# Performance work log

Hardware: AMD Instinct MI355X
Metric: run time of the kernel (lower is better)

Reference implementation:

```python
import jax, jax.numpy as jnp
import numpy as np

N_DIMS = 64
N_HALF = N_DIMS // 2
HIDDEN = 512
N_LAYERS = 8
BATCH = 16384

IDX_EVEN = np.arange(0, N_DIMS, 2)  # mask != 0 for even layers
IDX_ODD = np.arange(1, N_DIMS, 2)


def _init_mlp_params(key, n_in, n_hidden, n_out, n_layers):
    ks = jax.random.split(key, 3)
    def lin(k, fi, fo):
        return jax.random.normal(k, (n_layers, fi, fo), dtype=jnp.float32) / np.sqrt(fi)
    W1 = lin(ks[0], n_in, n_hidden)
    W2 = lin(ks[1], n_hidden, n_hidden)
    W3 = lin(ks[2], n_hidden, n_out)
    b1 = jnp.zeros((n_layers, n_hidden), jnp.float32)
    b2 = jnp.zeros((n_layers, n_hidden), jnp.float32)
    b3 = jnp.zeros((n_layers, n_out), jnp.float32)
    return W1, b1, W2, b2, W3, b3


def setup_inputs() -> dict:
    key = jax.random.key(0)
    ky, kt, ks = jax.random.split(key, 3)
    y = jax.random.normal(ky, (BATCH, N_DIMS), dtype=jnp.float32)
    tW1, tb1, tW2, tb2, tW3, tb3 = _init_mlp_params(kt, N_HALF, HIDDEN, N_HALF, N_LAYERS)
    sW1, sb1, sW2, sb2, sW3, sb3 = _init_mlp_params(ks, N_HALF, HIDDEN, N_HALF, N_LAYERS)
    s_scale = jnp.ones((N_LAYERS, N_HALF), jnp.float32)
    s_shift = jnp.zeros((N_LAYERS, N_HALF), jnp.float32)
    return {
        "y": y,
        "tW1": tW1, "tb1": tb1, "tW2": tW2, "tb2": tb2, "tW3": tW3, "tb3": tb3,
        "sW1": sW1, "sb1": sb1, "sW2": sW2, "sb2": sb2, "sW3": sW3, "sb3": sb3,
        "s_scale": s_scale, "s_shift": s_shift,
    }


def _mlp(x, W1, b1, W2, b2, W3, b3):
    h = jax.nn.relu(x @ W1 + b1)
    h = jax.nn.relu(h @ W2 + b2)
    return h @ W3 + b3


def reference(y, tW1, tb1, tW2, tb2, tW3, tb3,
              sW1, sb1, sW2, sb2, sW3, sb3, s_scale, s_shift):
    z = y
    log_det = jnp.zeros_like(y)
    for i in range(N_LAYERS):
        i0 = IDX_EVEN if i % 2 == 0 else IDX_ODD  # transformed half
        i1 = IDX_ODD if i % 2 == 0 else IDX_EVEN  # conditioning half
        z0 = z[:, i0]  # [B, 32]
        z1 = z[:, i1]  # [B, 32]
        t = _mlp(z1, tW1[i], tb1[i], tW2[i], tb2[i], tW3[i], tb3[i])
        s = jnp.tanh(_mlp(z1, sW1[i], sb1[i], sW2[i], sb2[i], sW3[i], sb3[i])) * s_scale[i] + s_shift[i]
        z0 = z0 * jnp.exp(s) + t
        z = z.at[:, i0].set(z0)
        log_det = log_det.at[:, i0].add(s)
    return z, log_det
```

## Files before the change

kernel.cpp:

```cpp
#include <hip/hip_runtime.h>

typedef unsigned short u16;
typedef unsigned int   u32;
typedef _Float16 f16;
typedef __attribute__((ext_vector_type(8))) _Float16 half8;
typedef __attribute__((ext_vector_type(4))) float f32x4;

#define NBATCH 16384

__device__ __forceinline__ u16 f2h(float x) {
  union { f16 h; u16 u; } v; v.h = (f16)x; return v.u;
}

__global__ __launch_bounds__(256) void cvt_all(
    const float* __restrict__ tW1, const float* __restrict__ sW1,
    const float* __restrict__ tW2, const float* __restrict__ sW2,
    const float* __restrict__ tW3, const float* __restrict__ sW3,
    u16* __restrict__ dW1, u16* __restrict__ dW2, u16* __restrict__ dW3)
{
  __shared__ float tile[32][33];
  const int z = blockIdx.z, bx = blockIdx.x;
  const float *tsrc, *ssrc; u16* dst; int M, N, nt, mt;
  if (bx < 16)       { tsrc = tW1; ssrc = sW1; dst = dW1; M = 32;  N = 512; nt = bx;           mt = 0; }
  else if (bx < 272) { tsrc = tW2; ssrc = sW2; dst = dW2; M = 512; N = 512; nt = (bx - 16) & 15; mt = (bx - 16) >> 4; }
  else               { tsrc = tW3; ssrc = sW3; dst = dW3; M = 512; N = 32;  nt = 0;            mt = bx - 272; }
  const float* src = ((z & 1) ? ssrc : tsrc) + (size_t)(z >> 1) * M * N;
  u16* d = dst + (size_t)z * M * N;
  const int n0 = nt * 32, m0 = mt * 32;
  for (int r = 0; r < 4; r++) {
    int m = m0 + threadIdx.y + r * 8, n = n0 + threadIdx.x;
    tile[threadIdx.y + r * 8][threadIdx.x] = src[(size_t)m * N + n];
  }
  __syncthreads();
  for (int r = 0; r < 4; r++) {
    int n = n0 + threadIdx.y + r * 8, m = m0 + threadIdx.x;
    d[(size_t)n * M + m] = f2h(tile[threadIdx.x][threadIdx.y + r * 8]);
  }
}

__global__ __launch_bounds__(512, 2) void meganvp(
    const float* __restrict__ y,
    const u16* __restrict__ W1T, const u16* __restrict__ W2T, const u16* __restrict__ W3T,
    const float* __restrict__ tb1, const float* __restrict__ sb1,
    const float* __restrict__ tb2, const float* __restrict__ sb2,
    const float* __restrict__ tb3, const float* __restrict__ sb3,
    const float* __restrict__ s_scale, const float* __restrict__ s_shift,
    float* __restrict__ out)
{
  __shared__ u16 bufA[64 * 512];
  __shared__ u16 bufB[64 * 512];
  __shared__ u16 X[64 * 40];
  __shared__ float TS[64 * 68];

  const int t = threadIdx.x;
  const int m0 = blockIdx.x * 64;
  const int lane = t & 63, w = t >> 6, lm = lane & 15, quad = lane >> 4;
  const int cw = w * 64;
  const int phase = blockIdx.x & 15;
  const int zr = t >> 3, zq = t & 7, c0 = zq * 8;

  float z[8], ld[8];
  {
    const float* yb = y + (size_t)(m0 + zr) * 64 + c0;
    f32x4 v0 = *(const f32x4*)&yb[0];
    f32x4 v1 = *(const f32x4*)&yb[4];
#pragma unroll
    for (int k = 0; k < 4; k++) { z[k] = v0[k]; z[4 + k] = v1[k]; }
#pragma unroll
    for (int e = 0; e < 8; e++) ld[e] = 0.f;
  }

  for (int layer = 0; layer < 8; layer++) {
    const int par = layer & 1;
    {
      union { u16 a[4]; uint2 v; } xv;
#pragma unroll
      for (int e = 0; e < 4; e++) xv.a[e] = f2h(z[2 * e + 1 - par]);
      *(uint2*)&X[zr * 40 + zq * 4] = xv.v;
    }
    __syncthreads();

    for (int net = 0; net < 2; net++) {
      const int idx = layer * 2 + net;

      {
        const float* b1p = (net ? sb1 : tb1) + layer * 512 + cw + quad * 4;
        f32x4 bias1[4];
#pragma unroll
        for (int ct = 0; ct < 4; ct++) bias1[ct] = *(const f32x4*)&b1p[ct * 16];
        const u16* W1p = W1T + ((size_t)idx * 512 + cw + lm) * 32 + quad * 8;
        half8 bv[4];
#pragma unroll
        for (int ct = 0; ct < 4; ct++) bv[ct] = *(const half8*)&W1p[ct * 512];
        half8 av[4];
#pragma unroll
        for (int rt = 0; rt < 4; rt++)
          av[rt] = *(const half8*)&X[(rt * 16 + lm) * 40 + quad * 8];
        f32x4 zz = {0.f, 0.f, 0.f, 0.f};
        f32x4 acc[4][4];
#pragma unroll
        for (int rt = 0; rt < 4; rt++)
#pragma unroll
          for (int ct = 0; ct < 4; ct++)
            acc[rt][ct] = __builtin_amdgcn_mfma_f32_16x16x32_f16(bv[ct], av[rt], zz, 0, 0, 0);
#pragma unroll
        for (int rt = 0; rt < 4; rt++) {
          const int m = rt * 16 + lm;
#pragma unroll
          for (int ct = 0; ct < 4; ct++) {
            const int n0 = cw + ct * 16 + quad * 4;
            union { u16 a[4]; uint2 v; } pk;
#pragma unroll
            for (int g = 0; g < 4; g++) {
              float v = acc[rt][ct][g] + bias1[ct][g];
              pk.a[g] = f2h(v > 0.f ? v : 0.f);
            }
            *(uint2*)&bufA[m * 512 + ((((n0 >> 3) ^ (m & 7)) << 3) | (n0 & 7))] = pk.v;
          }
        }
      }
      __syncthreads();

      {
        const float* b2p = (net ? sb2 : tb2) + layer * 512 + cw + quad * 4;
        f32x4 bias2[4];
#pragma unroll
        for (int ct = 0; ct < 4; ct++) bias2[ct] = *(const f32x4*)&b2p[ct * 16];
        const u16* W2p = W2T + ((size_t)idx * 512 + cw + lm) * 512 + quad * 8;
        f32x4 zz = {0.f, 0.f, 0.f, 0.f};
        f32x4 acc[4][4];
#pragma unroll
        for (int rt = 0; rt < 4; rt++)
#pragma unroll
          for (int ct = 0; ct < 4; ct++) acc[rt][ct] = zz;
        half8 bb[3][4];
#pragma unroll
        for (int p = 0; p < 3; p++) {
          const int kp = ((p + phase) & 15) * 32;
#pragma unroll
          for (int ct = 0; ct < 4; ct++)
            bb[p][ct] = *(const half8*)&W2p[ct * 8192 + kp];
        }
#pragma unroll
        for (int ci = 0; ci < 16; ci++) {
          const int kk = ((ci + phase) & 15) * 32;
          half8 av[4];
#pragma unroll
          for (int rt = 0; rt < 4; rt++) {
            const int m = rt * 16 + lm;
            av[rt] = *(const half8*)&bufA[m * 512 + ((((kk >> 3) + quad) ^ (m & 7)) << 3)];
          }
#pragma unroll
          for (int rt = 0; rt < 4; rt++)
#pragma unroll
            for (int ct = 0; ct < 4; ct++)
              acc[rt][ct] = __builtin_amdgcn_mfma_f32_16x16x32_f16(bb[ci % 3][ct], av[rt], acc[rt][ct], 0, 0, 0);
          if (ci < 13) {
            const int kn = ((ci + 3 + phase) & 15) * 32;
#pragma unroll
            for (int ct = 0; ct < 4; ct++)
              bb[ci % 3][ct] = *(const half8*)&W2p[ct * 8192 + kn];
          }
        }
#pragma unroll
        for (int rt = 0; rt < 4; rt++) {
          const int m = rt * 16 + lm;
#pragma unroll
          for (int ct = 0; ct < 4; ct++) {
            const int n0 = cw + ct * 16 + quad * 4;
            union { u16 a[4]; uint2 v; } pk;
#pragma unroll
            for (int g = 0; g < 4; g++) {
              float v = acc[rt][ct][g] + bias2[ct][g];
              pk.a[g] = f2h(v > 0.f ? v : 0.f);
            }
            *(uint2*)&bufB[m * 512 + ((((n0 >> 3) ^ (m & 7)) << 3) | (n0 & 7))] = pk.v;
          }
        }
      }
      __syncthreads();

      {
        const int hr = (w & 3) * 16, hc = (w >> 2) * 16;
        const u16* W3p = W3T + ((size_t)idx * 32 + hc + lm) * 512 + quad * 8;
        f32x4 ha[2];
        ha[0] = (f32x4){0.f, 0.f, 0.f, 0.f}; ha[1] = ha[0];
        const int m = hr + lm;
        half8 pv[4];
#pragma unroll
        for (int p = 0; p < 4; p++)
          pv[p] = *(const half8*)&W3p[((p + phase) & 15) * 32];
#pragma unroll
        for (int ci = 0; ci < 16; ci++) {
          const int kk = ((ci + phase) & 15) * 32;
          half8 av = *(const half8*)&bufB[m * 512 + ((((kk >> 3) + quad) ^ (m & 7)) << 3)];
          ha[ci & 1] = __builtin_amdgcn_mfma_f32_16x16x32_f16(pv[ci & 3], av, ha[ci & 1], 0, 0, 0);
          if (ci < 12)
            pv[ci & 3] = *(const half8*)&W3p[((ci + 4 + phase) & 15) * 32];
        }
        const int j0 = hc + quad * 4;
        if (net == 0) {
          const f32x4 b3 = *(const f32x4*)&tb3[layer * 32 + j0];
#pragma unroll
          for (int g = 0; g < 4; g++)
            TS[m * 68 + 2 * (j0 + g)] = ha[0][g] + ha[1][g] + b3[g];
        } else {
          const f32x4 b3 = *(const f32x4*)&sb3[layer * 32 + j0];
          const f32x4 sc = *(const f32x4*)&s_scale[layer * 32 + j0];
          const f32x4 sh = *(const f32x4*)&s_shift[layer * 32 + j0];
#pragma unroll
          for (int g = 0; g < 4; g++)
            TS[m * 68 + 2 * (j0 + g) + 1] = tanhf(ha[0][g] + ha[1][g] + b3[g]) * sc[g] + sh[g];
        }
      }
      __syncthreads();
    }

    {
      const float* base = &TS[zr * 68 + zq * 8];
      f32x4 q0 = *(const f32x4*)&base[0];
      f32x4 q1 = *(const f32x4*)&base[4];
      float q[8];
#pragma unroll
      for (int k = 0; k < 4; k++) { q[k] = q0[k]; q[4 + k] = q1[k]; }
#pragma unroll
      for (int e = 0; e < 4; e++) {
        const float tv = q[2 * e], sv = q[2 * e + 1];
        const int zi = 2 * e + par;
        z[zi] = z[zi] * expf(sv) + tv;
        ld[zi] += sv;
      }
    }
  }

  {
    float* zb = out + (size_t)(m0 + zr) * 64 + c0;
    float* lb = out + (size_t)NBATCH * 64 + (size_t)(m0 + zr) * 64 + c0;
    f32x4 v0, v1, l0, l1;
#pragma unroll
    for (int k = 0; k < 4; k++) {
      v0[k] = z[k]; v1[k] = z[4 + k];
      l0[k] = ld[k]; l1[k] = ld[4 + k];
    }
    *(f32x4*)&zb[0] = v0; *(f32x4*)&zb[4] = v1;
    *(f32x4*)&lb[0] = l0; *(f32x4*)&lb[4] = l1;
  }
}

extern "C" void kernel_launch(void* const* d_in, const int* in_sizes, int n_in,
                              void* d_out, int out_size, void* d_ws, size_t ws_size,
                              hipStream_t stream) {
  (void)in_sizes; (void)n_in; (void)out_size; (void)ws_size;
  const float* y   = (const float*)d_in[0];
  const float* tW1 = (const float*)d_in[1];
  const float* tb1 = (const float*)d_in[2];
  const float* tW2 = (const float*)d_in[3];
  const float* tb2 = (const float*)d_in[4];
  const float* tW3 = (const float*)d_in[5];
  const float* tb3 = (const float*)d_in[6];
  const float* sW1 = (const float*)d_in[7];
  const float* sb1 = (const float*)d_in[8];
  const float* sW2 = (const float*)d_in[9];
  const float* sb2 = (const float*)d_in[10];
  const float* sW3 = (const float*)d_in[11];
  const float* sb3 = (const float*)d_in[12];
  const float* s_scale = (const float*)d_in[13];
  const float* s_shift = (const float*)d_in[14];
  float* out = (float*)d_out;

  char* ws = (char*)d_ws;
  const size_t W1SZ = (size_t)16 * 512 * 32 * 2;
  const size_t W2SZ = (size_t)16 * 512 * 512 * 2;
  u16* W1 = (u16*)(ws);
  u16* W2 = (u16*)(ws + W1SZ);
  u16* W3 = (u16*)(ws + W1SZ + W2SZ);

  cvt_all<<<dim3(288, 1, 16), dim3(32, 8), 0, stream>>>(tW1, sW1, tW2, sW2, tW3, sW3,
                                                        W1, W2, W3);

  meganvp<<<256, 512, 0, stream>>>(y, W1, W2, W3, tb1, sb1, tb2, sb2, tb3, sb3,
                                   s_scale, s_shift, out);
}
```

Baseline: 436.3 us.

## Switch hidden-layer GEMMs to 32x32x16 MFMA and double-buffer LDS operand loads

Replaces the 16x16x32 MFMA tiling in the first two MLP layers with 32x32x16 MFMA tiles, which changes the register fragment layout, the bias indexing and the swizzled LDS writeback. The larger tile is meant to reduce the number of LDS operand reads per FLOP. The LDS activation loads in the second and third GEMMs are now prefetched one k-step ahead into double buffers so they overlap with the MFMAs. The larger f32x16 accumulators and the extra buffers raise register pressure, which could cause spills or lower occupancy under launch_bounds(512,2).

```diff
diff --git a/kernel.cpp b/kernel.cpp
--- a/kernel.cpp
+++ b/kernel.cpp
@@ -5,6 +5,7 @@
 typedef _Float16 f16;
 typedef __attribute__((ext_vector_type(8))) _Float16 half8;
 typedef __attribute__((ext_vector_type(4))) float f32x4;
+typedef __attribute__((ext_vector_type(16))) float f32x16;
 
 #define NBATCH 16384
 
@@ -55,6 +56,7 @@
   const int t = threadIdx.x;
   const int m0 = blockIdx.x * 64;
   const int lane = t & 63, w = t >> 6, lm = lane & 15, quad = lane >> 4;
+  const int l31 = lane & 31, lh = lane >> 5;
   const int cw = w * 64;
   const int phase = blockIdx.x & 15;
   const int zr = t >> 3, zq = t & 7, c0 = zq * 8;
@@ -84,98 +86,129 @@
       const int idx = layer * 2 + net;
 
       {
-        const float* b1p = (net ? sb1 : tb1) + layer * 512 + cw + quad * 4;
-        f32x4 bias1[4];
-#pragma unroll
-        for (int ct = 0; ct < 4; ct++) bias1[ct] = *(const f32x4*)&b1p[ct * 16];
-        const u16* W1p = W1T + ((size_t)idx * 512 + cw + lm) * 32 + quad * 8;
-        half8 bv[4];
-#pragma unroll
-        for (int ct = 0; ct < 4; ct++) bv[ct] = *(const half8*)&W1p[ct * 512];
-        half8 av[4];
-#pragma unroll
-        for (int rt = 0; rt < 4; rt++)
-          av[rt] = *(const half8*)&X[(rt * 16 + lm) * 40 + quad * 8];
-        f32x4 zz = {0.f, 0.f, 0.f, 0.f};
-        f32x4 acc[4][4];
-#pragma unroll
-        for (int rt = 0; rt < 4; rt++)
-#pragma unroll
-          for (int ct = 0; ct < 4; ct++)
-            acc[rt][ct] = __builtin_amdgcn_mfma_f32_16x16x32_f16(bv[ct], av[rt], zz, 0, 0, 0);
-#pragma unroll
-        for (int rt = 0; rt < 4; rt++) {
-          const int m = rt * 16 + lm;
-#pragma unroll
-          for (int ct = 0; ct < 4; ct++) {
-            const int n0 = cw + ct * 16 + quad * 4;
-            union { u16 a[4]; uint2 v; } pk;
-#pragma unroll
-            for (int g = 0; g < 4; g++) {
-              float v = acc[rt][ct][g] + bias1[ct][g];
-              pk.a[g] = f2h(v > 0.f ? v : 0.f);
+        const u16* W1p = W1T + ((size_t)idx * 512 + cw + l31) * 32 + lh * 8;
+        half8 wv[2][2], xv[2][2];
+#pragma unroll
+        for (int ct = 0; ct < 2; ct++)
+#pragma unroll
+          for (int kh = 0; kh < 2; kh++)
+            wv[ct][kh] = *(const half8*)&W1p[ct * 1024 + kh * 16];
+#pragma unroll
+        for (int rt = 0; rt < 2; rt++)
+#pragma unroll
+          for (int kh = 0; kh < 2; kh++)
+            xv[rt][kh] = *(const half8*)&X[(rt * 32 + l31) * 40 + kh * 16 + lh * 8];
+        f32x16 zz;
+#pragma unroll
+        for (int i = 0; i < 16; i++) zz[i] = 0.f;
+        f32x16 acc1[2][2];
+#pragma unroll
+        for (int rt = 0; rt < 2; rt++)
+#pragma unroll
+          for (int ct = 0; ct < 2; ct++) {
+            acc1[rt][ct] = __builtin_amdgcn_mfma_f32_32x32x16_f16(wv[ct][0], xv[rt][0], zz, 0, 0, 0);
+            acc1[rt][ct] = __builtin_amdgcn_mfma_f32_32x32x16_f16(wv[ct][1], xv[rt][1], acc1[rt][ct], 0, 0, 0);
+          }
+        const float* b1g = (net ? sb1 : tb1) + layer * 512;
+#pragma unroll
+        for (int rt = 0; rt < 2; rt++) {
+          const int m = rt * 32 + l31;
+#pragma unroll
+          for (int ct = 0; ct < 2; ct++)
+#pragma unroll
+            for (int g8 = 0; g8 < 4; g8++) {
+              const int n0 = cw + ct * 32 + lh * 4 + g8 * 8;
+              const f32x4 bias = *(const f32x4*)&b1g[n0];
+              union { u16 a[4]; uint2 v; } pk;
+#pragma unroll
+              for (int g = 0; g < 4; g++) {
+                float v = acc1[rt][ct][g8 * 4 + g] + bias[g];
+                pk.a[g] = f2h(v > 0.f ? v : 0.f);
+              }
+              *(uint2*)&bufA[m * 512 + ((((n0 >> 3) ^ (m & 7)) << 3) | (n0 & 7))] = pk.v;
             }
-            *(uint2*)&bufA[m * 512 + ((((n0 >> 3) ^ (m & 7)) << 3) | (n0 & 7))] = pk.v;
-          }
         }
       }
       __syncthreads();
 
       {
-        const float* b2p = (net ? sb2 : tb2) + layer * 512 + cw + quad * 4;
-        f32x4 bias2[4];
-#pragma unroll
-        for (int ct = 0; ct < 4; ct++) bias2[ct] = *(const f32x4*)&b2p[ct * 16];
-        const u16* W2p = W2T + ((size_t)idx * 512 + cw + lm) * 512 + quad * 8;
-        f32x4 zz = {0.f, 0.f, 0.f, 0.f};
-        f32x4 acc[4][4];
-#pragma unroll
-        for (int rt = 0; rt < 4; rt++)
-#pragma unroll
-          for (int ct = 0; ct < 4; ct++) acc[rt][ct] = zz;
+        const u16* W2p = W2T + ((size_t)idx * 512 + cw + l31) * 512 + lh * 8;
+        f32x16 acc[2][2];
+#pragma unroll
+        for (int rt = 0; rt < 2; rt++)
+#pragma unroll
+          for (int ct = 0; ct < 2; ct++)
+#pragma unroll
+            for (int i = 0; i < 16; i++) acc[rt][ct][i] = 0.f;
         half8 bb[3][4];
 #pragma unroll
         for (int p = 0; p < 3; p++) {
           const int kp = ((p + phase) & 15) * 32;
 #pragma unroll
-          for (int ct = 0; ct < 4; ct++)
-            bb[p][ct] = *(const half8*)&W2p[ct * 8192 + kp];
+          for (int ct = 0; ct < 2; ct++)
+#pragma unroll
+            for (int kh = 0; kh < 2; kh++)
+              bb[p][ct * 2 + kh] = *(const half8*)&W2p[ct * 16384 + kp + kh * 16];
+        }
+        half8 av[2][4];
+        {
+          const int kk0 = (phase & 15) * 32;
+#pragma unroll
+          for (int rt = 0; rt < 2; rt++)
+#pragma unroll
+            for (int kh = 0; kh < 2; kh++) {
+              const int m = rt * 32 + l31;
+              const int c = (kk0 >> 3) + kh * 2 + lh;
+              av[0][rt * 2 + kh] = *(const half8*)&bufA[m * 512 + ((c ^ (m & 7)) << 3)];
+            }
         }
 #pragma unroll
         for (int ci = 0; ci < 16; ci++) {
-          const int kk = ((ci + phase) & 15) * 32;
-          half8 av[4];
-#pragma unroll
-          for (int rt = 0; rt < 4; rt++) {
-            const int m = rt * 16 + lm;
-            av[rt] = *(const half8*)&bufA[m * 512 + ((((kk >> 3) + quad) ^ (m & 7)) << 3)];
+          if (ci < 15) {
+            const int kk1 = ((ci + 1 + phase) & 15) * 32;
+#pragma unroll
+            for (int rt = 0; rt < 2; rt++)
+#pragma unroll
+              for (int kh = 0; kh < 2; kh++) {
+                const int m = rt * 32 + l31;
+                const int c = (kk1 >> 3) + kh * 2 + lh;
+                av[(ci + 1) & 1][rt * 2 + kh] = *(const half8*)&bufA[m * 512 + ((c ^ (m & 7)) << 3)];
+              }
           }
 #pragma unroll
-          for (int rt = 0; rt < 4; rt++)
-#pragma unroll
-            for (int ct = 0; ct < 4; ct++)
-              acc[rt][ct] = __builtin_amdgcn_mfma_f32_16x16x32_f16(bb[ci % 3][ct], av[rt], acc[rt][ct], 0, 0, 0);
+          for (int rt = 0; rt < 2; rt++)
+#pragma unroll
+            for (int ct = 0; ct < 2; ct++) {
+              acc[rt][ct] = __builtin_amdgcn_mfma_f32_32x32x16_f16(bb[ci % 3][ct * 2 + 0], av[ci & 1][rt * 2 + 0], acc[rt][ct], 0, 0, 0);
+              acc[rt][ct] = __builtin_amdgcn_mfma_f32_32x32x16_f16(bb[ci % 3][ct * 2 + 1], av[ci & 1][rt * 2 + 1], acc[rt][ct], 0, 0, 0);
+            }
           if (ci < 13) {
             const int kn = ((ci + 3 + phase) & 15) * 32;
 #pragma unroll
-            for (int ct = 0; ct < 4; ct++)
-              bb[ci % 3][ct] = *(const half8*)&W2p[ct * 8192 + kn];
+            for (int ct = 0; ct < 2; ct++)
+#pragma unroll
+              for (int kh = 0; kh < 2; kh++)
+                bb[ci % 3][ct * 2 + kh] = *(const half8*)&W2p[ct * 16384 + kn + kh * 16];
           }
         }
-#pragma unroll
-        for (int rt = 0; rt < 4; rt++) {
-          const int m = rt * 16 + lm;
-#pragma unroll
-          for (int ct = 0; ct < 4; ct++) {
-            const int n0 = cw + ct * 16 + quad * 4;
-            union { u16 a[4]; uint2 v; } pk;
-#pragma unroll
-            for (int g = 0; g < 4; g++) {
-              float v = acc[rt][ct][g] + bias2[ct][g];
-              pk.a[g] = f2h(v > 0.f ? v : 0.f);
+        const float* b2g = (net ? sb2 : tb2) + layer * 512;
+#pragma unroll
+        for (int rt = 0; rt < 2; rt++) {
+          const int m = rt * 32 + l31;
+#pragma unroll
+          for (int ct = 0; ct < 2; ct++)
+#pragma unroll
+            for (int g8 = 0; g8 < 4; g8++) {
+              const int n0 = cw + ct * 32 + lh * 4 + g8 * 8;
+              const f32x4 bias = *(const f32x4*)&b2g[n0];
+              union { u16 a[4]; uint2 v; } pk;
+#pragma unroll
+              for (int g = 0; g < 4; g++) {
+                float v = acc[rt][ct][g8 * 4 + g] + bias[g];
+                pk.a[g] = f2h(v > 0.f ? v : 0.f);
+              }
+              *(uint2*)&bufB[m * 512 + ((((n0 >> 3) ^ (m & 7)) << 3) | (n0 & 7))] = pk.v;
             }
-            *(uint2*)&bufB[m * 512 + ((((n0 >> 3) ^ (m & 7)) << 3) | (n0 & 7))] = pk.v;
-          }
         }
       }
       __syncthreads();
@@ -190,11 +223,18 @@
 #pragma unroll
         for (int p = 0; p < 4; p++)
           pv[p] = *(const half8*)&W3p[((p + phase) & 15) * 32];
+        half8 avh[2];
+        {
+          const int kk0 = (phase & 15) * 32;
+          avh[0] = *(const half8*)&bufB[m * 512 + ((((kk0 >> 3) + quad) ^ (m & 7)) << 3)];
+        }
 #pragma unroll
         for (int ci = 0; ci < 16; ci++) {
-          const int kk = ((ci + phase) & 15) * 32;
-          half8 av = *(const half8*)&bufB[m * 512 + ((((kk >> 3) + quad) ^ (m & 7)) << 3)];
-          ha[ci & 1] = __builtin_amdgcn_mfma_f32_16x16x32_f16(pv[ci & 3], av, ha[ci & 1], 0, 0, 0);
+          if (ci < 15) {
+            const int kk1 = ((ci + 1 + phase) & 15) * 32;
+            avh[(ci + 1) & 1] = *(const half8*)&bufB[m * 512 + ((((kk1 >> 3) + quad) ^ (m & 7)) << 3)];
+          }
+          ha[ci & 1] = __builtin_amdgcn_mfma_f32_16x16x32_f16(pv[ci & 3], avh[ci & 1], ha[ci & 1], 0, 0, 0);
           if (ci < 12)
             pv[ci & 3] = *(const half8*)&W3p[((ci + 4 + phase) & 15) * 32];
         }
```

Result: slower. 463.3 us (+6.2%).

## Prefetch next-stage weights before barriers and fuse head with next net's first layer

Applied to the files above, without the earlier changes.

Restructures the per-layer schedule so the W2 and W3 register prefetches are issued before each barrier, letting global loads overlap the sync wait. The t-net head is merged with the s-net first hidden layer in one barrier phase, removing one __syncthreads per layer. Biases are folded into the MFMA accumulator initialisation instead of being added afterwards. The cost is higher register pressure from the prefetch buffers staying live across phases, which could lower occupancy or cause spills.

```diff
diff --git a/kernel.cpp b/kernel.cpp
--- a/kernel.cpp
+++ b/kernel.cpp
@@ -58,6 +58,7 @@
   const int cw = w * 64;
   const int phase = blockIdx.x & 15;
   const int zr = t >> 3, zq = t & 7, c0 = zq * 8;
+  const int hr = (w & 3) * 16, hc = (w >> 2) * 16;
 
   float z[8], ld[8];
   {
@@ -70,6 +71,142 @@
     for (int e = 0; e < 8; e++) ld[e] = 0.f;
   }
 
+  half8 bb[3][4];
+  half8 pv[4];
+
+  auto BBPREF = [&](int idx) {
+    const u16* W2p = W2T + ((size_t)idx * 512 + cw + lm) * 512 + quad * 8;
+#pragma unroll
+    for (int p = 0; p < 3; p++) {
+      const int kp = ((p + phase) & 15) * 32;
+#pragma unroll
+      for (int ct = 0; ct < 4; ct++)
+        bb[p][ct] = *(const half8*)&W2p[ct * 8192 + kp];
+    }
+  };
+  auto PVPREF = [&](int idx) {
+    const u16* W3p = W3T + ((size_t)idx * 32 + hc + lm) * 512 + quad * 8;
+#pragma unroll
+    for (int p = 0; p < 4; p++)
+      pv[p] = *(const half8*)&W3p[((p + phase) & 15) * 32];
+  };
+
+  auto H1 = [&](int layer, int net) {
+    const int idx = layer * 2 + net;
+    const float* b1p = (net ? sb1 : tb1) + layer * 512 + cw + quad * 4;
+    f32x4 bias1[4];
+#pragma unroll
+    for (int ct = 0; ct < 4; ct++) bias1[ct] = *(const f32x4*)&b1p[ct * 16];
+    const u16* W1p = W1T + ((size_t)idx * 512 + cw + lm) * 32 + quad * 8;
+    half8 bv[4];
+#pragma unroll
+    for (int ct = 0; ct < 4; ct++) bv[ct] = *(const half8*)&W1p[ct * 512];
+    half8 av[4];
+#pragma unroll
+    for (int rt = 0; rt < 4; rt++)
+      av[rt] = *(const half8*)&X[(rt * 16 + lm) * 40 + quad * 8];
+    f32x4 acc[4][4];
+#pragma unroll
+    for (int rt = 0; rt < 4; rt++)
+#pragma unroll
+      for (int ct = 0; ct < 4; ct++)
+        acc[rt][ct] = __builtin_amdgcn_mfma_f32_16x16x32_f16(bv[ct], av[rt], bias1[ct], 0, 0, 0);
+#pragma unroll
+    for (int rt = 0; rt < 4; rt++) {
+      const int m = rt * 16 + lm;
+#pragma unroll
+      for (int ct = 0; ct < 4; ct++) {
+        const int n0 = cw + ct * 16 + quad * 4;
+        union { u16 a[4]; uint2 v; } pk;
+#pragma unroll
+        for (int g = 0; g < 4; g++) {
+          float v = acc[rt][ct][g];
+          pk.a[g] = f2h(v > 0.f ? v : 0.f);
+        }
+        *(uint2*)&bufA[m * 512 + ((((n0 >> 3) ^ (m & 7)) << 3) | (n0 & 7))] = pk.v;
+      }
+    }
+  };
+
+  auto H2 = [&](int layer, int net) {
+    const int idx = layer * 2 + net;
+    const float* b2p = (net ? sb2 : tb2) + layer * 512 + cw + quad * 4;
+    f32x4 acc[4][4];
+#pragma unroll
+    for (int ct = 0; ct < 4; ct++) {
+      const f32x4 b = *(const f32x4*)&b2p[ct * 16];
+#pragma unroll
+      for (int rt = 0; rt < 4; rt++) acc[rt][ct] = b;
+    }
+    const u16* W2p = W2T + ((size_t)idx * 512 + cw + lm) * 512 + quad * 8;
+#pragma unroll
+    for (int ci = 0; ci < 16; ci++) {
+      const int kk = ((ci + phase) & 15) * 32;
+      half8 av[4];
+#pragma unroll
+      for (int rt = 0; rt < 4; rt++) {
+        const int m = rt * 16 + lm;
+        av[rt] = *(const half8*)&bufA[m * 512 + ((((kk >> 3) + quad) ^ (m & 7)) << 3)];
+      }
+#pragma unroll
+      for (int rt = 0; rt < 4; rt++)
+#pragma unroll
+        for (int ct = 0; ct < 4; ct++)
+          acc[rt][ct] = __builtin_amdgcn_mfma_f32_16x16x32_f16(bb[ci % 3][ct], av[rt], acc[rt][ct], 0, 0, 0);
+      if (ci < 13) {
+        const int kn = ((ci + 3 + phase) & 15) * 32;
+#pragma unroll
+        for (int ct = 0; ct < 4; ct++)
+          bb[ci % 3][ct] = *(const half8*)&W2p[ct * 8192 + kn];
+      }
+    }
+#pragma unroll
+    for (int rt = 0; rt < 4; rt++) {
+      const int m = rt * 16 + lm;
+#pragma unroll
+      for (int ct = 0; ct < 4; ct++) {
+        const int n0 = cw + ct * 16 + quad * 4;
+        union { u16 a[4]; uint2 v; } pk;
+#pragma unroll
+        for (int g = 0; g < 4; g++) {
+          float v = acc[rt][ct][g];
+          pk.a[g] = f2h(v > 0.f ? v : 0.f);
+        }
+        *(uint2*)&bufB[m * 512 + ((((n0 >> 3) ^ (m & 7)) << 3) | (n0 & 7))] = pk.v;
+      }
+    }
+  };
+
+  auto HEAD = [&](int layer, int net) {
+    const int idx = layer * 2 + net;
+    const u16* W3p = W3T + ((size_t)idx * 32 + hc + lm) * 512 + quad * 8;
+    const int j0 = hc + quad * 4;
+    f32x4 ha[2];
+    ha[0] = net ? *(const f32x4*)&sb3[layer * 32 + j0]
+                : *(const f32x4*)&tb3[layer * 32 + j0];
+    ha[1] = (f32x4){0.f, 0.f, 0.f, 0.f};
+    const int m = hr + lm;
+#pragma unroll
+    for (int ci = 0; ci < 16; ci++) {
+      const int kk = ((ci + phase) & 15) * 32;
+      half8 av = *(const half8*)&bufB[m * 512 + ((((kk >> 3) + quad) ^ (m & 7)) << 3)];
+      ha[ci & 1] = __builtin_amdgcn_mfma_f32_16x16x32_f16(pv[ci & 3], av, ha[ci & 1], 0, 0, 0);
+      if (ci < 12)
+        pv[ci & 3] = *(const half8*)&W3p[((ci + 4 + phase) & 15) * 32];
+    }
+    if (net == 0) {
+#pragma unroll
+      for (int g = 0; g < 4; g++)
+        TS[m * 68 + 2 * (j0 + g)] = ha[0][g] + ha[1][g];
+    } else {
+      const f32x4 sc = *(const f32x4*)&s_scale[layer * 32 + j0];
+      const f32x4 sh = *(const f32x4*)&s_shift[layer * 32 + j0];
+#pragma unroll
+      for (int g = 0; g < 4; g++)
+        TS[m * 68 + 2 * (j0 + g) + 1] = tanhf(ha[0][g] + ha[1][g]) * sc[g] + sh[g];
+    }
+  };
+
   for (int layer = 0; layer < 8; layer++) {
     const int par = layer & 1;
     {
@@ -80,141 +217,25 @@
     }
     __syncthreads();
 
-    for (int net = 0; net < 2; net++) {
-      const int idx = layer * 2 + net;
-
-      {
-        const float* b1p = (net ? sb1 : tb1) + layer * 512 + cw + quad * 4;
-        f32x4 bias1[4];
-#pragma unroll
-        for (int ct = 0; ct < 4; ct++) bias1[ct] = *(const f32x4*)&b1p[ct * 16];
-        const u16* W1p = W1T + ((size_t)idx * 512 + cw + lm) * 32 + quad * 8;
-        half8 bv[4];
-#pragma unroll
-        for (int ct = 0; ct < 4; ct++) bv[ct] = *(const half8*)&W1p[ct * 512];
-        half8 av[4];
-#pragma unroll
-        for (int rt = 0; rt < 4; rt++)
-          av[rt] = *(const half8*)&X[(rt * 16 + lm) * 40 + quad * 8];
-        f32x4 zz = {0.f, 0.f, 0.f, 0.f};
-        f32x4 acc[4][4];
-#pragma unroll
-        for (int rt = 0; rt < 4; rt++)
-#pragma unroll
-          for (int ct = 0; ct < 4; ct++)
-            acc[rt][ct] = __builtin_amdgcn_mfma_f32_16x16x32_f16(bv[ct], av[rt], zz, 0, 0, 0);
-#pragma unroll
-        for (int rt = 0; rt < 4; rt++) {
-          const int m = rt * 16 + lm;
-#pragma unroll
-          for (int ct = 0; ct < 4; ct++) {
-            const int n0 = cw + ct * 16 + quad * 4;
-            union { u16 a[4]; uint2 v; } pk;
-#pragma unroll
-            for (int g = 0; g < 4; g++) {
-              float v = acc[rt][ct][g] + bias1[ct][g];
-              pk.a[g] = f2h(v > 0.f ? v : 0.f);
-            }
-            *(uint2*)&bufA[m * 512 + ((((n0 >> 3) ^ (m & 7)) << 3) | (n0 & 7))] = pk.v;
-          }
-        }
-      }
-      __syncthreads();
-
-      {
-        const float* b2p = (net ? sb2 : tb2) + layer * 512 + cw + quad * 4;
-        f32x4 bias2[4];
-#pragma unroll
-        for (int ct = 0; ct < 4; ct++) bias2[ct] = *(const f32x4*)&b2p[ct * 16];
-        const u16* W2p = W2T + ((size_t)idx * 512 + cw + lm) * 512 + quad * 8;
-        f32x4 zz = {0.f, 0.f, 0.f, 0.f};
-        f32x4 acc[4][4];
-#pragma unroll
-        for (int rt = 0; rt < 4; rt++)
-#pragma unroll
-          for (int ct = 0; ct < 4; ct++) acc[rt][ct] = zz;
-        half8 bb[3][4];
-#pragma unroll
-        for (int p = 0; p < 3; p++) {
-          const int kp = ((p + phase) & 15) * 32;
-#pragma unroll
-          for (int ct = 0; ct < 4; ct++)
-            bb[p][ct] = *(const half8*)&W2p[ct * 8192 + kp];
-        }
-#pragma unroll
-        for (int ci = 0; ci < 16; ci++) {
-          const int kk = ((ci + phase) & 15) * 32;
-          half8 av[4];
-#pragma unroll
-          for (int rt = 0; rt < 4; rt++) {
-            const int m = rt * 16 + lm;
-            av[rt] = *(const half8*)&bufA[m * 512 + ((((kk >> 3) + quad) ^ (m & 7)) << 3)];
-          }
-#pragma unroll
-          for (int rt = 0; rt < 4; rt++)
-#pragma unroll
-            for (int ct = 0; ct < 4; ct++)
-              acc[rt][ct] = __builtin_amdgcn_mfma_f32_16x16x32_f16(bb[ci % 3][ct], av[rt], acc[rt][ct], 0, 0, 0);
-          if (ci < 13) {
-            const int kn = ((ci + 3 + phase) & 15) * 32;
-#pragma unroll
-            for (int ct = 0; ct < 4; ct++)
-              bb[ci % 3][ct] = *(const half8*)&W2p[ct * 8192 + kn];
-          }
-        }
-#pragma unroll
-        for (int rt = 0; rt < 4; rt++) {
-          const int m = rt * 16 + lm;
-#pragma unroll
-          for (int ct = 0; ct < 4; ct++) {
-            const int n0 = cw + ct * 16 + quad * 4;
-            union { u16 a[4]; uint2 v; } pk;
-#pragma unroll
-            for (int g = 0; g < 4; g++) {
-              float v = acc[rt][ct][g] + bias2[ct][g];
-              pk.a[g] = f2h(v > 0.f ? v : 0.f);
-            }
-            *(uint2*)&bufB[m * 512 + ((((n0 >> 3) ^ (m & 7)) << 3) | (n0 & 7))] = pk.v;
-          }
-        }
-      }
-      __syncthreads();
-
-      {
-        const int hr = (w & 3) * 16, hc = (w >> 2) * 16;
-        const u16* W3p = W3T + ((size_t)idx * 32 + hc + lm) * 512 + quad * 8;
-        f32x4 ha[2];
-        ha[0] = (f32x4){0.f, 0.f, 0.f, 0.f}; ha[1] = ha[0];
-        const int m = hr + lm;
-        half8 pv[4];
-#pragma unroll
-        for (int p = 0; p < 4; p++)
-          pv[p] = *(const half8*)&W3p[((p + phase) & 15) * 32];
-#pragma unroll
-        for (int ci = 0; ci < 16; ci++) {
-          const int kk = ((ci + phase) & 15) * 32;
-          half8 av = *(const half8*)&bufB[m * 512 + ((((kk >> 3) + quad) ^ (m & 7)) << 3)];
-          ha[ci & 1] = __builtin_amdgcn_mfma_f32_16x16x32_f16(pv[ci & 3], av, ha[ci & 1], 0, 0, 0);
-          if (ci < 12)
-            pv[ci & 3] = *(const half8*)&W3p[((ci + 4 + phase) & 15) * 32];
-        }
-        const int j0 = hc + quad * 4;
-        if (net == 0) {
-          const f32x4 b3 = *(const f32x4*)&tb3[layer * 32 + j0];
-#pragma unroll
-          for (int g = 0; g < 4; g++)
-            TS[m * 68 + 2 * (j0 + g)] = ha[0][g] + ha[1][g] + b3[g];
-        } else {
-          const f32x4 b3 = *(const f32x4*)&sb3[layer * 32 + j0];
-          const f32x4 sc = *(const f32x4*)&s_scale[layer * 32 + j0];
-          const f32x4 sh = *(const f32x4*)&s_shift[layer * 32 + j0];
-#pragma unroll
-          for (int g = 0; g < 4; g++)
-            TS[m * 68 + 2 * (j0 + g) + 1] = tanhf(ha[0][g] + ha[1][g] + b3[g]) * sc[g] + sh[g];
-        }
-      }
-      __syncthreads();
-    }
+    H1(layer, 0);
+    BBPREF(layer * 2 + 0);
+    __syncthreads();
+
+    H2(layer, 0);
+    PVPREF(layer * 2 + 0);
+    __syncthreads();
+
+    HEAD(layer, 0);
+    H1(layer, 1);
+    BBPREF(layer * 2 + 1);
+    __syncthreads();
+
+    H2(layer, 1);
+    PVPREF(layer * 2 + 1);
+    __syncthreads();
+
+    HEAD(layer, 1);
+    __syncthreads();
 
     {
       const float* base = &TS[zr * 68 + zq * 8];
```

Result: slower. 500.4 us (+14.7%).
